# Performance work log

Measured on AMD Instinct MI355X. Metric: run time of the kernel, lower is better.

The kernel has to match this reference:

```python
import jax, jax.numpy as jnp
import numpy as np

N, E = 50000, 800000
IN, HID, H, OUT = 128, 32, 4, 40
K_SAMPLE, EPS_K = 25.0, 1e-3  # fixed k=25 (no dp_budget), compute_beta eps


def _glorot(key, shape):
    fan_in, fan_out = shape[0], shape[-1]
    lim = jnp.sqrt(6.0 / (fan_in + fan_out))
    return jax.random.uniform(key, shape, jnp.float32, -lim, lim)


def setup_inputs() -> dict:
    key = jax.random.key(0)
    ks = jax.random.split(key, 16)
    x = jax.random.normal(ks[0], (N, IN), jnp.float32)
    edge_index = jax.random.randint(ks[1], (2, E), 0, N, jnp.int64)
    # layer 0: IN -> (H, HID)
    W0 = _glorot(ks[2], (IN, H * HID)); as0 = _glorot(ks[3], (H, HID)); ad0 = _glorot(ks[4], (H, HID)); b0 = jnp.zeros((H * HID,), jnp.float32)
    # layer 1: H*HID -> (H, HID)
    W1 = _glorot(ks[5], (H * HID, H * HID)); as1 = _glorot(ks[6], (H, HID)); ad1 = _glorot(ks[7], (H, HID)); b1 = jnp.zeros((H * HID,), jnp.float32)
    # layer 2: H*HID -> (1, OUT)
    W2 = _glorot(ks[8], (H * HID, OUT)); as2 = _glorot(ks[9], (1, OUT)); ad2 = _glorot(ks[10], (1, OUT)); b2 = jnp.zeros((OUT,), jnp.float32)
    # BatchNorm affine params (batch-stat mode, deterministic)
    g_bn0 = jnp.ones((H * HID,), jnp.float32); be_bn0 = jnp.zeros((H * HID,), jnp.float32)
    g_bn1 = jnp.ones((H * HID,), jnp.float32); be_bn1 = jnp.zeros((H * HID,), jnp.float32)
    return {"x": x, "edge_index": edge_index,
            "W0": W0, "as0": as0, "ad0": ad0, "b0": b0,
            "W1": W1, "as1": as1, "ad1": ad1, "b1": b1,
            "W2": W2, "as2": as2, "ad2": ad2, "b2": b2,
            "g_bn0": g_bn0, "be_bn0": be_bn0, "g_bn1": g_bn1, "be_bn1": be_bn1}


def gat_conv(x, src, dst, W, a_src, a_dst, bias, heads, d_out):
    # PyG GATConv, add_self_loops=False, concat over heads
    h = (x @ W).reshape(-1, heads, d_out)                       # [N,H,D]
    al_s = jnp.sum(h * a_src, axis=-1)                          # [N,H]
    al_d = jnp.sum(h * a_dst, axis=-1)                          # [N,H]
    e = jax.nn.leaky_relu(al_s[src] + al_d[dst], 0.2)           # [E,H]
    m = jax.ops.segment_max(e, dst, num_segments=N)
    m = jnp.where(jnp.isfinite(m), m, 0.0)                      # guard empty segments
    p = jnp.exp(e - m[dst])
    s = jax.ops.segment_sum(p, dst, num_segments=N)
    alpha = p / (s[dst] + 1e-16)                                # segment softmax over incoming edges
    out = jax.ops.segment_sum(alpha[:, :, None] * h[src], dst, num_segments=N)  # [N,H,D]
    return out.reshape(-1, heads * d_out) + bias


def batch_norm(x, gamma, beta):
    mu = jnp.mean(x, axis=0)
    var = jnp.mean(jnp.square(x - mu), axis=0)
    return gamma * (x - mu) * jax.lax.rsqrt(var + 1e-5) + beta


def beta_scale(l):
    return 1.0 + 1.0 / (l + 1.0) * (1.0 / (K_SAMPLE + EPS_K))


def reference(x, edge_index, W0, as0, ad0, b0, W1, as1, ad1, b1, W2, as2, ad2, b2,
              g_bn0, be_bn0, g_bn1, be_bn1):
    src, dst = edge_index[0], edge_index[1]
    h = gat_conv(x, src, dst, W0, as0, ad0, b0, H, HID)
    h = jax.nn.elu(batch_norm(h, g_bn0, be_bn0)) * beta_scale(0)
    h = gat_conv(h, src, dst, W1, as1, ad1, b1, H, HID)
    h = jax.nn.elu(batch_norm(h, g_bn1, be_bn1)) * beta_scale(1)
    h = gat_conv(h, src, dst, W2, as2, ad2, b2, 1, OUT)
    return jax.nn.log_softmax(h, axis=1)
```

## Files before the change

### kernel.cpp

```cpp
#include <hip/hip_runtime.h>
#include <math.h>

#define N_NODES 50000
#define N_EDGES 800000
#define DIN 128
#define DHID 128
#define NH 4
#define HID 32
#define DOUT 40

#define PB 128
#define NPB 391

typedef __fp16 fp16x2 __attribute__((ext_vector_type(2)));

static __device__ __forceinline__ float lrelu(float x) { return x > 0.f ? x : 0.2f * x; }

static __device__ __forceinline__ unsigned int pkh(float a, float b) {
    union { fp16x2 h2; unsigned int u; } cv;
    cv.h2 = __builtin_amdgcn_cvt_pkrtz(a, b);
    return cv.u;
}
static __device__ __forceinline__ unsigned short f2h(float a) {
    union { _Float16 h; unsigned short s; } cv;
    cv.h = (_Float16)a;
    return cv.s;
}

static __device__ __forceinline__ void fma8(float* acc, uint4 w, float p) {
    union { unsigned int u; _Float16 h[2]; } c0, c1, c2, c3;
    c0.u = w.x; c1.u = w.y; c2.u = w.z; c3.u = w.w;
    acc[0] = fmaf((float)c0.h[0], p, acc[0]);
    acc[1] = fmaf((float)c0.h[1], p, acc[1]);
    acc[2] = fmaf((float)c1.h[0], p, acc[2]);
    acc[3] = fmaf((float)c1.h[1], p, acc[3]);
    acc[4] = fmaf((float)c2.h[0], p, acc[4]);
    acc[5] = fmaf((float)c2.h[1], p, acc[5]);
    acc[6] = fmaf((float)c3.h[0], p, acc[6]);
    acc[7] = fmaf((float)c3.h[1], p, acc[7]);
}

static __device__ __forceinline__ float4 bnelu4(float4 x, float4 sc, float4 sh, float bs) {
    float y0 = fmaf(x.x, sc.x, sh.x);
    float y1 = fmaf(x.y, sc.y, sh.y);
    float y2 = fmaf(x.z, sc.z, sh.z);
    float y3 = fmaf(x.w, sc.w, sh.w);
    y0 = (y0 > 0.f ? y0 : __expf(y0) - 1.f) * bs;
    y1 = (y1 > 0.f ? y1 : __expf(y1) - 1.f) * bs;
    y2 = (y2 > 0.f ? y2 : __expf(y2) - 1.f) * bs;
    y3 = (y3 > 0.f ? y3 : __expf(y3) - 1.f) * bs;
    return {y0, y1, y2, y3};
}

__global__ __launch_bounds__(256) void bucket_hist_kernel(const int* __restrict__ dstv, int* __restrict__ bhist) {
    __shared__ int h[PB];
    if (threadIdx.x < PB) h[threadIdx.x] = 0;
    __syncthreads();
    for (int i = blockIdx.x * blockDim.x + threadIdx.x; i < N_EDGES; i += gridDim.x * blockDim.x)
        atomicAdd(&h[(unsigned)dstv[i] / NPB], 1);
    __syncthreads();
    if (threadIdx.x < PB) atomicAdd(&bhist[threadIdx.x], h[threadIdx.x]);
}

__global__ __launch_bounds__(128) void bucket_scan_kernel(const int* __restrict__ bhist,
                                                          int* __restrict__ bucket_base, int* __restrict__ cursor) {
    __shared__ int sA[PB], sB[PB];
    int t = threadIdx.x;
    sA[t] = bhist[t];
    __syncthreads();
    int* s = sA; int* d2 = sB;
    for (int off = 1; off < PB; off <<= 1) {
        d2[t] = s[t] + (t >= off ? s[t - off] : 0);
        __syncthreads();
        int* tmp = s; s = d2; d2 = tmp;
    }
    int excl = s[t] - bhist[t];
    bucket_base[t] = excl;
    cursor[t] = excl;
    if (t == PB - 1) bucket_base[PB] = s[t];
}

__global__ __launch_bounds__(256) void partition_kernel(const int* __restrict__ srcv, const int* __restrict__ dstv,
                                                        int* __restrict__ cursor, uint2* __restrict__ part) {
    __shared__ uint2 rec[2048];
    __shared__ int cnt[PB], lofs[PB], gbase[PB];
    __shared__ int sA[PB], sB[PB];
    __shared__ int tot_s;
    const int t = threadIdx.x;
    const int base0 = blockIdx.x * 4096;
    for (int round = 0; round < 2; ++round) {
        int rbase = base0 + round * 2048;
        if (t < PB) cnt[t] = 0;
        __syncthreads();
        int myb[8]; int myr[8]; uint2 myrec[8];
#pragma unroll
        for (int i = 0; i < 8; ++i) {
            int e = rbase + i * 256 + t;
            bool valid = e < N_EDGES;
            int sv = valid ? srcv[e] : 0;
            int dv = valid ? dstv[e] : 0;
            myrec[i].x = (unsigned)sv;
            myrec[i].y = (unsigned)dv;
            int b = (unsigned)dv / NPB;
            myb[i] = valid ? b : -1;
            myr[i] = valid ? atomicAdd(&cnt[b], 1) : 0;
        }
        __syncthreads();
        if (t < PB) sA[t] = cnt[t];
        __syncthreads();
        int* s = sA; int* d2 = sB;
        for (int off = 1; off < PB; off <<= 1) {
            if (t < PB) d2[t] = s[t] + (t >= off ? s[t - off] : 0);
            __syncthreads();
            int* tmp = s; s = d2; d2 = tmp;
        }
        if (t < PB) {
            int c = cnt[t];
            lofs[t] = s[t] - c;
            gbase[t] = c > 0 ? atomicAdd(&cursor[t], c) : 0;
            if (t == PB - 1) tot_s = s[t];
        }
        __syncthreads();
#pragma unroll
        for (int i = 0; i < 8; ++i)
            if (myb[i] >= 0) rec[lofs[myb[i]] + myr[i]] = myrec[i];
        __syncthreads();
        int tot = tot_s;
#pragma unroll
        for (int i = 0; i < 8; ++i) {
            int lp = i * 256 + t;
            if (lp < tot) {
                uint2 r = rec[lp];
                int b = r.y / NPB;
                part[gbase[b] + (lp - lofs[b])] = r;
            }
        }
        __syncthreads();
    }
}

__global__ __launch_bounds__(256) void bucket_csr_kernel(const uint2* __restrict__ part, const int* __restrict__ bucket_base,
                                                         int* __restrict__ row_ptr, int* __restrict__ csr_src) {
    __shared__ int hist[512], sA[512], sB[512], cur[NPB];
    const int b = blockIdx.x, t = threadIdx.x;
    const int base = bucket_base[b];
    const int n = bucket_base[b + 1] - base;
    hist[t] = 0; hist[t + 256] = 0;
    __syncthreads();
    for (int i = t; i < n; i += 256)
        atomicAdd(&hist[part[base + i].y - b * NPB], 1);
    __syncthreads();
    sA[t] = hist[t]; sA[t + 256] = hist[t + 256];
    __syncthreads();
    int* s = sA; int* d2 = sB;
    for (int off = 1; off < 512; off <<= 1) {
        d2[t] = s[t] + (t >= off ? s[t - off] : 0);
        int u = t + 256;
        d2[u] = s[u] + (u >= off ? s[u - off] : 0);
        __syncthreads();
        int* tmp = s; s = d2; d2 = tmp;
    }
    for (int j = t; j < NPB; j += 256) {
        int node = b * NPB + j;
        int excl = s[j] - hist[j];
        if (node < N_NODES) row_ptr[node] = base + excl;
        cur[j] = excl;
    }
    if (b == PB - 1 && t == 0) row_ptr[N_NODES] = N_EDGES;
    __syncthreads();
    for (int i = t; i < n; i += 256) {
        uint2 r = part[base + i];
        int loc = r.y - b * NPB;
        int p = atomicAdd(&cur[loc], 1);
        csr_src[base + p] = (int)r.x;
    }
}

__global__ __launch_bounds__(256) void gemm128_kernel(
    const float* __restrict__ X, const float* __restrict__ W,
    const float* __restrict__ a_src, const float* __restrict__ a_dst,
    const float* __restrict__ scale, const float* __restrict__ shift, float bscale, int apply_bn,
    unsigned int* __restrict__ Hout, float* __restrict__ als, float* __restrict__ ald) {
    __shared__ float Xs[32][68];
    __shared__ float Ws[32][64];
    const int t = threadIdx.x;
    const int tx = t & 15, ty = t >> 4;
    const int r0 = (blockIdx.x >> 1) * 64;
    const int c0 = (blockIdx.x & 1) * 64;
    const int sr = t >> 2, sa = t & 3;
    const int wk = t >> 4, wc = (t & 15) * 4;

    int gr = r0 + sr; gr = gr < N_NODES ? gr : N_NODES - 1;
    const float* Xrow = X + (size_t)gr * 128;
    float4 xpreA = *(const float4*)(Xrow + 8 * sa);
    float4 xpreB = *(const float4*)(Xrow + 8 * sa + 4);
    if (apply_bn) {
        xpreA = bnelu4(xpreA, *(const float4*)(scale + 8 * sa), *(const float4*)(shift + 8 * sa), bscale);
        xpreB = bnelu4(xpreB, *(const float4*)(scale + 8 * sa + 4), *(const float4*)(shift + 8 * sa + 4), bscale);
    }
    float4 wpreA = *(const float4*)(W + (size_t)wk * 128 + c0 + wc);
    float4 wpreB = *(const float4*)(W + (size_t)(wk + 16) * 128 + c0 + wc);

    float acc[4][4];
#pragma unroll
    for (int i = 0; i < 4; ++i)
#pragma unroll
        for (int c = 0; c < 4; ++c) acc[i][c] = 0.f;

    for (int step = 0; step < 4; ++step) {
        __syncthreads();
        Xs[8 * sa + 0][sr] = xpreA.x;
        Xs[8 * sa + 1][sr] = xpreA.y;
        Xs[8 * sa + 2][sr] = xpreA.z;
        Xs[8 * sa + 3][sr] = xpreA.w;
        Xs[8 * sa + 4][sr] = xpreB.x;
        Xs[8 * sa + 5][sr] = xpreB.y;
        Xs[8 * sa + 6][sr] = xpreB.z;
        Xs[8 * sa + 7][sr] = xpreB.w;
        *(float4*)&Ws[wk][wc] = wpreA;
        *(float4*)&Ws[wk + 16][wc] = wpreB;
        if (step < 3) {
            int k0 = (step + 1) * 32;
            xpreA = *(const float4*)(Xrow + k0 + 8 * sa);
            xpreB = *(const float4*)(Xrow + k0 + 8 * sa + 4);
            if (apply_bn) {
                xpreA = bnelu4(xpreA, *(const float4*)(scale + k0 + 8 * sa), *(const float4*)(shift + k0 + 8 * sa), bscale);
                xpreB = bnelu4(xpreB, *(const float4*)(scale + k0 + 8 * sa + 4), *(const float4*)(shift + k0 + 8 * sa + 4), bscale);
            }
            wpreA = *(const float4*)(W + (size_t)(k0 + wk) * 128 + c0 + wc);
            wpreB = *(const float4*)(W + (size_t)(k0 + wk + 16) * 128 + c0 + wc);
        }
        __syncthreads();
#pragma unroll
        for (int kk = 0; kk < 32; ++kk) {
            float4 xv = *(const float4*)&Xs[kk][4 * ty];
            float4 wv = *(const float4*)&Ws[kk][4 * tx];
            float xr[4] = {xv.x, xv.y, xv.z, xv.w};
            float wr[4] = {wv.x, wv.y, wv.z, wv.w};
#pragma unroll
            for (int i = 0; i < 4; ++i)
#pragma unroll
                for (int c = 0; c < 4; ++c)
                    acc[i][c] = fmaf(xr[i], wr[c], acc[i][c]);
        }
    }
    const int head = (c0 >> 5) + (tx >> 3);
    float asv[4], adv[4];
#pragma unroll
    for (int c = 0; c < 4; ++c) {
        asv[c] = a_src[(head & 1) * 32 + (4 * tx + c) % 32 + (head >> 1) * 64];
        adv[c] = a_dst[(head & 1) * 32 + (4 * tx + c) % 32 + (head >> 1) * 64];
    }
#pragma unroll
    for (int i = 0; i < 4; ++i) {
        int r = r0 + 4 * ty + i;
        bool valid = r < N_NODES;
        if (valid) {
            uint2 pk = {pkh(acc[i][0], acc[i][1]), pkh(acc[i][2], acc[i][3])};
            *(uint2*)(Hout + (size_t)r * 64 + (c0 >> 1) + 2 * tx) = pk;
        }
        float ps = 0.f, pd = 0.f;
#pragma unroll
        for (int c = 0; c < 4; ++c) {
            ps = fmaf(acc[i][c], asv[c], ps);
            pd = fmaf(acc[i][c], adv[c], pd);
        }
#pragma unroll
        for (int off = 1; off < 8; off <<= 1) {
            ps += __shfl_xor(ps, off);
            pd += __shfl_xor(pd, off);
        }
        if (valid && (tx & 7) == 0) {
            als[r * 4 + head] = ps;
            ald[r * 4 + head] = pd;
        }
    }
}

__global__ __launch_bounds__(256) void gemm40_kernel(
    const float* __restrict__ X, const float* __restrict__ W,
    const float* __restrict__ a_src, const float* __restrict__ a_dst,
    const float* __restrict__ scale, const float* __restrict__ shift, float bscale,
    unsigned short* __restrict__ Hout, float* __restrict__ als, float* __restrict__ ald) {
    __shared__ float Xs[64][36];
    __shared__ float Ws[40][36];
    const int t = threadIdx.x;
    const int tx = t & 7, ty = t >> 3;
    const int r0 = blockIdx.x * 64;
    const int sr = t >> 2, sa = t & 3;

    int gr = r0 + sr; gr = gr < N_NODES ? gr : N_NODES - 1;
    const float* Xrow = X + (size_t)gr * 128;
    float4 xpreA = bnelu4(*(const float4*)(Xrow + 8 * sa),
                          *(const float4*)(scale + 8 * sa), *(const float4*)(shift + 8 * sa), bscale);
    float4 xpreB = bnelu4(*(const float4*)(Xrow + 8 * sa + 4),
                          *(const float4*)(scale + 8 * sa + 4), *(const float4*)(shift + 8 * sa + 4), bscale);
    float wpre[5];
#pragma unroll
    for (int i = 0; i < 5; ++i) wpre[i] = W[t + 256 * i];

    float acc[2][5];
#pragma unroll
    for (int i = 0; i < 2; ++i)
#pragma unroll
        for (int j = 0; j < 5; ++j) acc[i][j] = 0.f;

    for (int step = 0; step < 4; ++step) {
        __syncthreads();
        *(float4*)&Xs[sr][8 * sa] = xpreA;
        *(float4*)&Xs[sr][8 * sa + 4] = xpreB;
#pragma unroll
        for (int i = 0; i < 5; ++i) {
            int idx = t + 256 * i;
            Ws[idx % 40][idx / 40] = wpre[i];
        }
        if (step < 3) {
            int k0 = (step + 1) * 32;
            xpreA = bnelu4(*(const float4*)(Xrow + k0 + 8 * sa),
                           *(const float4*)(scale + k0 + 8 * sa), *(const float4*)(shift + k0 + 8 * sa), bscale);
            xpreB = bnelu4(*(const float4*)(Xrow + k0 + 8 * sa + 4),
                           *(const float4*)(scale + k0 + 8 * sa + 4), *(const float4*)(shift + k0 + 8 * sa + 4), bscale);
#pragma unroll
            for (int i = 0; i < 5; ++i) wpre[i] = W[k0 * 40 + t + 256 * i];
        }
        __syncthreads();
#pragma unroll
        for (int kk4 = 0; kk4 < 8; ++kk4) {
            float4 xa = *(const float4*)&Xs[2 * ty][4 * kk4];
            float4 xb = *(const float4*)&Xs[2 * ty + 1][4 * kk4];
#pragma unroll
            for (int j = 0; j < 5; ++j) {
                float4 wv = *(const float4*)&Ws[tx + 8 * j][4 * kk4];
                acc[0][j] = fmaf(xa.x, wv.x, acc[0][j]);
                acc[0][j] = fmaf(xa.y, wv.y, acc[0][j]);
                acc[0][j] = fmaf(xa.z, wv.z, acc[0][j]);
                acc[0][j] = fmaf(xa.w, wv.w, acc[0][j]);
                acc[1][j] = fmaf(xb.x, wv.x, acc[1][j]);
                acc[1][j] = fmaf(xb.y, wv.y, acc[1][j]);
                acc[1][j] = fmaf(xb.z, wv.z, acc[1][j]);
                acc[1][j] = fmaf(xb.w, wv.w, acc[1][j]);
            }
        }
    }
    float asv[5], adv[5];
#pragma unroll
    for (int j = 0; j < 5; ++j) {
        asv[j] = a_src[tx + 8 * j];
        adv[j] = a_dst[tx + 8 * j];
    }
#pragma unroll
    for (int i = 0; i < 2; ++i) {
        int r = r0 + 2 * ty + i;
        bool valid = r < N_NODES;
        if (valid) {
#pragma unroll
            for (int j = 0; j < 5; ++j)
                Hout[(size_t)r * 40 + tx + 8 * j] = f2h(acc[i][j]);
        }
        float ps = 0.f, pd = 0.f;
#pragma unroll
        for (int j = 0; j < 5; ++j) {
            ps = fmaf(acc[i][j], asv[j], ps);
            pd = fmaf(acc[i][j], adv[j], pd);
        }
#pragma unroll
        for (int off = 1; off < 8; off <<= 1) {
            ps += __shfl_xor(ps, off);
            pd += __shfl_xor(pd, off);
        }
        if (valid && tx == 0) {
            als[r] = ps;
            ald[r] = pd;
        }
    }
}

__global__ __launch_bounds__(256) void agg128_kernel(
    const int* __restrict__ row_ptr, const int* __restrict__ csr_src,
    const unsigned int* __restrict__ Ht, const float* __restrict__ als, const float* __restrict__ ald,
    const float* __restrict__ bias, float* __restrict__ out) {
    __shared__ float s_p[4][256];
    __shared__ int s_u[4][64];
    int v = (blockIdx.x * blockDim.x + threadIdx.x) >> 6;
    v = __builtin_amdgcn_readfirstlane(v);
    int lane = threadIdx.x & 63;
    int wslot = threadIdx.x >> 6;
    if (v >= N_NODES) return;
    int beg = row_ptr[v], end = row_ptr[v + 1];
    float4 ad4 = *(const float4*)(ald + (size_t)v * 4);
    const int g = lane >> 4;
    const int li = lane & 15;
    const int hh = li >> 2;
    float tsum = 0.f;
    float acc[8];
#pragma unroll
    for (int j = 0; j < 8; ++j) acc[j] = 0.f;

    for (int cbeg = beg; cbeg < end; cbeg += 64) {
        int cnt = min(64, end - cbeg);
        bool act = lane < cnt;
        int u = act ? csr_src[cbeg + lane] : 0;
        float p0, p1, p2, p3;
        if (act) {
            float4 s4 = *(const float4*)(als + (size_t)u * 4);
            p0 = __expf(lrelu(s4.x + ad4.x));
            p1 = __expf(lrelu(s4.y + ad4.y));
            p2 = __expf(lrelu(s4.z + ad4.z));
            p3 = __expf(lrelu(s4.w + ad4.w));
        } else {
            p0 = p1 = p2 = p3 = 0.f;
        }
        s_u[wslot][lane] = u;
        float4 pv = {p0, p1, p2, p3};
        *(float4*)&s_p[wslot][lane * 4] = pv;
        for (int i = 0; i < cnt; i += 4) {
            int e = i + g;
            int uu = s_u[wslot][e];
            float p = s_p[wslot][e * 4 + hh];
            uint4 w4 = *(const uint4*)(Ht + (size_t)uu * 64 + li * 4);
            tsum += p;
            fma8(acc, w4, p);
        }
    }
#pragma unroll
    for (int j = 0; j < 8; ++j) {
        acc[j] += __shfl_xor(acc[j], 16);
        acc[j] += __shfl_xor(acc[j], 32);
    }
    tsum += __shfl_xor(tsum, 16);
    tsum += __shfl_xor(tsum, 32);
    float inv = 1.f / (tsum + 1e-16f);
    if (g == 0) {
        float4 b0 = *(const float4*)(bias + 8 * li);
        float4 b1 = *(const float4*)(bias + 8 * li + 4);
        float4 o0 = {acc[0] * inv + b0.x, acc[1] * inv + b0.y, acc[2] * inv + b0.z, acc[3] * inv + b0.w};
        float4 o1 = {acc[4] * inv + b1.x, acc[5] * inv + b1.y, acc[6] * inv + b1.z, acc[7] * inv + b1.w};
        *(float4*)(out + (size_t)v * DHID + 8 * li) = o0;
        *(float4*)(out + (size_t)v * DHID + 8 * li + 4) = o1;
    }
}

__global__ __launch_bounds__(256) void agg40_kernel(
    const int* __restrict__ row_ptr, const int* __restrict__ csr_src,
    const unsigned int* __restrict__ HtU, const float* __restrict__ als, const float* __restrict__ ald,
    const float* __restrict__ bias, float* __restrict__ out) {
    __shared__ float s_p[4][64];
    __shared__ int s_u[4][64];
    int v = (blockIdx.x * blockDim.x + threadIdx.x) >> 6;
    v = __builtin_amdgcn_readfirstlane(v);
    int lane = threadIdx.x & 63;
    int wslot = threadIdx.x >> 6;
    if (v >= N_NODES) return;
    int beg = row_ptr[v], end = row_ptr[v + 1];
    float adv = ald[v];
    const int g = lane >> 5;
    const int li = lane & 31;
    const bool own = li < 20;
    float tsum = 0.f;
    float a0 = 0.f, a1 = 0.f;
    for (int cbeg = beg; cbeg < end; cbeg += 64) {
        int cnt = min(64, end - cbeg);
        bool act = lane < cnt;
        int u = act ? csr_src[cbeg + lane] : 0;
        float p = act ? __expf(lrelu(als[u] + adv)) : 0.f;
        s_u[wslot][lane] = u;
        s_p[wslot][lane] = p;
        for (int i = 0; i < cnt; i += 2) {
            int e2 = i + g;
            int uu = s_u[wslot][e2];
            float pp = s_p[wslot][e2];
            unsigned int w = own ? HtU[(size_t)uu * 20 + li] : 0u;
            union { unsigned int u; _Float16 h[2]; } cv;
            cv.u = w;
            tsum += pp;
            a0 = fmaf((float)cv.h[0], pp, a0);
            a1 = fmaf((float)cv.h[1], pp, a1);
        }
    }
    a0 += __shfl_xor(a0, 32);
    a1 += __shfl_xor(a1, 32);
    tsum += __shfl_xor(tsum, 32);
    float inv = 1.f / (tsum + 1e-16f);
    float z0 = own ? (a0 * inv + bias[2 * li]) : -1e30f;
    float z1 = own ? (a1 * inv + bias[2 * li + 1]) : -1e30f;
    float zm = fmaxf(z0, z1);
#pragma unroll
    for (int off = 1; off < 32; off <<= 1) zm = fmaxf(zm, __shfl_xor(zm, off));
    float se = own ? (__expf(z0 - zm) + __expf(z1 - zm)) : 0.f;
#pragma unroll
    for (int off = 1; off < 32; off <<= 1) se += __shfl_xor(se, off);
    float ls = zm + logf(se);
    if (own && g == 0) {
        float2 o = {z0 - ls, z1 - ls};
        *(float2*)(out + (size_t)v * DOUT + 2 * li) = o;
    }
}

__global__ __launch_bounds__(256) void bn_stats_kernel(const float* __restrict__ X,
                                                       float* __restrict__ sums, float* __restrict__ sqs) {
    int f = threadIdx.x & 127;
    int sub = threadIdx.x >> 7;
    int rbeg = blockIdx.x * 100;
    float s = 0.f, q = 0.f;
    for (int r = rbeg + sub; r < rbeg + 100; r += 2) {
        float x = X[(size_t)r * DHID + f];
        s += x;
        q += x * x;
    }
    __shared__ float ls[256], lq[256];
    ls[threadIdx.x] = s;
    lq[threadIdx.x] = q;
    __syncthreads();
    if (threadIdx.x < 128) {
        s = ls[threadIdx.x] + ls[threadIdx.x + 128];
        q = lq[threadIdx.x] + lq[threadIdx.x + 128];
        atomicAdd(&sums[f], s);
        atomicAdd(&sqs[f], q);
    }
}

__global__ void bn_finalize_kernel(const float* __restrict__ sums, const float* __restrict__ sqs,
                                   const float* __restrict__ gamma, const float* __restrict__ beta,
                                   float* __restrict__ scale, float* __restrict__ shift) {
    int f = threadIdx.x;
    if (f < DHID) {
        float mu = sums[f] * (1.f / N_NODES);
        float var = sqs[f] * (1.f / N_NODES) - mu * mu;
        float sc = gamma[f] * rsqrtf(var + 1e-5f);
        scale[f] = sc;
        shift[f] = beta[f] - mu * sc;
    }
}

extern "C" void kernel_launch(void* const* d_in, const int* in_sizes, int n_in,
                              void* d_out, int out_size, void* d_ws, size_t ws_size,
                              hipStream_t stream) {
    (void)in_sizes; (void)n_in; (void)out_size; (void)ws_size;
    const float* x = (const float*)d_in[0];
    const int* ei = (const int*)d_in[1];
    const float* W0 = (const float*)d_in[2];
    const float* as0 = (const float*)d_in[3];
    const float* ad0 = (const float*)d_in[4];
    const float* b0 = (const float*)d_in[5];
    const float* W1 = (const float*)d_in[6];
    const float* as1 = (const float*)d_in[7];
    const float* ad1 = (const float*)d_in[8];
    const float* b1 = (const float*)d_in[9];
    const float* W2 = (const float*)d_in[10];
    const float* as2 = (const float*)d_in[11];
    const float* ad2 = (const float*)d_in[12];
    const float* b2 = (const float*)d_in[13];
    const float* g_bn0 = (const float*)d_in[14];
    const float* be_bn0 = (const float*)d_in[15];
    const float* g_bn1 = (const float*)d_in[16];
    const float* be_bn1 = (const float*)d_in[17];
    float* out = (float*)d_out;

    const int* srcv = ei;
    const int* dstv = ei + N_EDGES;

    char* p = (char*)d_ws;
    auto carve = [&](size_t bytes) {
        char* q = p;
        p += (bytes + 255) & ~(size_t)255;
        return q;
    };
    unsigned int* h_bf = (unsigned int*)carve((size_t)N_NODES * 64 * 4);
    float* agg   = (float*)carve((size_t)N_NODES * DHID * 4);
    float* als   = (float*)carve((size_t)N_NODES * NH * 4);
    float* ald   = (float*)carve((size_t)N_NODES * NH * 4);
    int* row_ptr = (int*)carve((size_t)(N_NODES + 1) * 4);
    int* csr_src = (int*)carve((size_t)N_EDGES * 4);
    uint2* part  = (uint2*)carve((size_t)N_EDGES * 8);
    int* bhist   = (int*)carve(PB * 4);
    int* bucket_base = (int*)carve((PB + 1) * 4);
    int* cursor  = (int*)carve(PB * 4);
    float* sums  = (float*)carve(256 * 4);
    float* sqs   = sums + 128;
    float* scale = (float*)carve(DHID * 4);
    float* shift = (float*)carve(DHID * 4);

    const float bs0 = 1.0f + 1.0f / 25.001f;
    const float bs1 = 1.0f + 0.5f / 25.001f;

    const int RT64 = (N_NODES + 63) / 64;
    const int G128B = RT64 * 2;
    const int G40B = RT64;
    const int AB = (N_NODES * 64 + 255) / 256;
    const int PARTB = (N_EDGES + 4095) / 4096;

    hipMemsetAsync(bhist, 0, PB * 4, stream);
    bucket_hist_kernel<<<400, 256, 0, stream>>>(dstv, bhist);
    bucket_scan_kernel<<<1, PB, 0, stream>>>(bhist, bucket_base, cursor);
    partition_kernel<<<PARTB, 256, 0, stream>>>(srcv, dstv, cursor, part);
    bucket_csr_kernel<<<PB, 256, 0, stream>>>(part, bucket_base, row_ptr, csr_src);

    gemm128_kernel<<<G128B, 256, 0, stream>>>(x, W0, as0, ad0, nullptr, nullptr, 1.f, 0, h_bf, als, ald);
    agg128_kernel<<<AB, 256, 0, stream>>>(row_ptr, csr_src, h_bf, als, ald, b0, agg);
    hipMemsetAsync(sums, 0, 256 * 4, stream);
    bn_stats_kernel<<<500, 256, 0, stream>>>(agg, sums, sqs);
    bn_finalize_kernel<<<1, 128, 0, stream>>>(sums, sqs, g_bn0, be_bn0, scale, shift);

    gemm128_kernel<<<G128B, 256, 0, stream>>>(agg, W1, as1, ad1, scale, shift, bs0, 1, h_bf, als, ald);
    agg128_kernel<<<AB, 256, 0, stream>>>(row_ptr, csr_src, h_bf, als, ald, b1, agg);
    hipMemsetAsync(sums, 0, 256 * 4, stream);
    bn_stats_kernel<<<500, 256, 0, stream>>>(agg, sums, sqs);
    bn_finalize_kernel<<<1, 128, 0, stream>>>(sums, sqs, g_bn1, be_bn1, scale, shift);

    gemm40_kernel<<<G40B, 256, 0, stream>>>(agg, W2, as2, ad2, scale, shift, bs1, (unsigned short*)h_bf, als, ald);
    agg40_kernel<<<AB, 256, 0, stream>>>(row_ptr, csr_src, h_bf, als, ald, b2, out);
}
```

Before: 302.2 us.

## Fuse scan and BN finalize via last-block pattern, widen agg40 gathers to uint4

The bucket histogram now runs the prefix scan in whichever block finishes last, and BN stats compute scale/shift the same way from per-block partials. This removes several small kernel launches and memsets, and the float atomics in BN stats become plain stores of partials. agg40 now has 12 edge groups of 5 lanes, each loading a uint4 (8 halves), and reduces the groups through shared memory. In exchange it adds a serial 500-block reduction in one block and a shared-memory reduction at the end of agg40.

```diff
diff --git a/kernel.cpp b/kernel.cpp
--- a/kernel.cpp
+++ b/kernel.cpp
@@ -11,6 +11,7 @@
 
 #define PB 128
 #define NPB 391
+#define BN_BLOCKS 500
 
 typedef __fp16 fp16x2 __attribute__((ext_vector_type(2)));
 
@@ -52,32 +53,40 @@
     return {y0, y1, y2, y3};
 }
 
-__global__ __launch_bounds__(256) void bucket_hist_kernel(const int* __restrict__ dstv, int* __restrict__ bhist) {
+__global__ __launch_bounds__(256) void bucket_hist_scan_kernel(
+    const int* __restrict__ dstv, int* __restrict__ bhist, int* __restrict__ counter,
+    int* __restrict__ bucket_base, int* __restrict__ cursor) {
     __shared__ int h[PB];
-    if (threadIdx.x < PB) h[threadIdx.x] = 0;
-    __syncthreads();
-    for (int i = blockIdx.x * blockDim.x + threadIdx.x; i < N_EDGES; i += gridDim.x * blockDim.x)
+    const int t = threadIdx.x;
+    if (t < PB) h[t] = 0;
+    __syncthreads();
+    for (int i = blockIdx.x * blockDim.x + t; i < N_EDGES; i += gridDim.x * blockDim.x)
         atomicAdd(&h[(unsigned)dstv[i] / NPB], 1);
     __syncthreads();
-    if (threadIdx.x < PB) atomicAdd(&bhist[threadIdx.x], h[threadIdx.x]);
-}
-
-__global__ __launch_bounds__(128) void bucket_scan_kernel(const int* __restrict__ bhist,
-                                                          int* __restrict__ bucket_base, int* __restrict__ cursor) {
-    __shared__ int sA[PB], sB[PB];
-    int t = threadIdx.x;
-    sA[t] = bhist[t];
-    __syncthreads();
-    int* s = sA; int* d2 = sB;
-    for (int off = 1; off < PB; off <<= 1) {
-        d2[t] = s[t] + (t >= off ? s[t - off] : 0);
-        __syncthreads();
-        int* tmp = s; s = d2; d2 = tmp;
-    }
-    int excl = s[t] - bhist[t];
-    bucket_base[t] = excl;
-    cursor[t] = excl;
-    if (t == PB - 1) bucket_base[PB] = s[t];
+    if (t < PB) atomicAdd(&bhist[t], h[t]);
+    __threadfence();
+    __shared__ int done_s;
+    __syncthreads();
+    if (t == 0) done_s = atomicAdd(counter, 1);
+    __syncthreads();
+    if (done_s == gridDim.x - 1) {
+        __threadfence();
+        __shared__ int sA[PB], sB[PB];
+        if (t < PB) sA[t] = bhist[t];
+        __syncthreads();
+        int* s = sA; int* d2 = sB;
+        for (int off = 1; off < PB; off <<= 1) {
+            if (t < PB) d2[t] = s[t] + (t >= off ? s[t - off] : 0);
+            __syncthreads();
+            int* tmp = s; s = d2; d2 = tmp;
+        }
+        if (t < PB) {
+            int excl = s[t] - bhist[t];
+            bucket_base[t] = excl;
+            cursor[t] = excl;
+            if (t == PB - 1) bucket_base[PB] = s[t];
+        }
+    }
 }
 
 __global__ __launch_bounds__(256) void partition_kernel(const int* __restrict__ srcv, const int* __restrict__ dstv,
@@ -442,10 +451,11 @@
 
 __global__ __launch_bounds__(256) void agg40_kernel(
     const int* __restrict__ row_ptr, const int* __restrict__ csr_src,
-    const unsigned int* __restrict__ HtU, const float* __restrict__ als, const float* __restrict__ ald,
+    const uint4* __restrict__ Ht4, const float* __restrict__ als, const float* __restrict__ ald,
     const float* __restrict__ bias, float* __restrict__ out) {
-    __shared__ float s_p[4][64];
-    __shared__ int s_u[4][64];
+    __shared__ float s_p[4][76];
+    __shared__ int s_u[4][76];
+    __shared__ float s_red[4][12][41];
     int v = (blockIdx.x * blockDim.x + threadIdx.x) >> 6;
     v = __builtin_amdgcn_readfirstlane(v);
     int lane = threadIdx.x & 63;
@@ -453,11 +463,15 @@
     if (v >= N_NODES) return;
     int beg = row_ptr[v], end = row_ptr[v + 1];
     float adv = ald[v];
-    const int g = lane >> 5;
-    const int li = lane & 31;
-    const bool own = li < 20;
+    const int g = lane / 5;
+    const int li = lane - g * 5;
+    const bool gact = lane < 60;
+    if (lane < 12) { s_u[wslot][64 + lane] = 0; s_p[wslot][64 + lane] = 0.f; }
     float tsum = 0.f;
-    float a0 = 0.f, a1 = 0.f;
+    float a[8];
+#pragma unroll
+    for (int j = 0; j < 8; ++j) a[j] = 0.f;
+
     for (int cbeg = beg; cbeg < end; cbeg += 64) {
         int cnt = min(64, end - cbeg);
         bool act = lane < cnt;
@@ -465,41 +479,47 @@
         float p = act ? __expf(lrelu(als[u] + adv)) : 0.f;
         s_u[wslot][lane] = u;
         s_p[wslot][lane] = p;
-        for (int i = 0; i < cnt; i += 2) {
-            int e2 = i + g;
-            int uu = s_u[wslot][e2];
-            float pp = s_p[wslot][e2];
-            unsigned int w = own ? HtU[(size_t)uu * 20 + li] : 0u;
-            union { unsigned int u; _Float16 h[2]; } cv;
-            cv.u = w;
-            tsum += pp;
-            a0 = fmaf((float)cv.h[0], pp, a0);
-            a1 = fmaf((float)cv.h[1], pp, a1);
-        }
-    }
-    a0 += __shfl_xor(a0, 32);
-    a1 += __shfl_xor(a1, 32);
-    tsum += __shfl_xor(tsum, 32);
-    float inv = 1.f / (tsum + 1e-16f);
-    float z0 = own ? (a0 * inv + bias[2 * li]) : -1e30f;
-    float z1 = own ? (a1 * inv + bias[2 * li + 1]) : -1e30f;
-    float zm = fmaxf(z0, z1);
-#pragma unroll
-    for (int off = 1; off < 32; off <<= 1) zm = fmaxf(zm, __shfl_xor(zm, off));
-    float se = own ? (__expf(z0 - zm) + __expf(z1 - zm)) : 0.f;
-#pragma unroll
-    for (int off = 1; off < 32; off <<= 1) se += __shfl_xor(se, off);
+        for (int i = 0; i < cnt; i += 12) {
+            int e = i + g;
+            int uu = s_u[wslot][e];
+            float pp = s_p[wslot][e];
+            uint4 w = {0u, 0u, 0u, 0u};
+            if (gact) w = Ht4[(size_t)uu * 5 + li];
+            if (gact) tsum += pp;
+            fma8(a, w, pp);
+        }
+    }
+    if (gact) {
+#pragma unroll
+        for (int j = 0; j < 8; ++j) s_red[wslot][g][li * 8 + j] = a[j];
+        if (li == 0) s_red[wslot][g][40] = tsum;
+    }
+    bool fown = lane < DOUT;
+    float accf = 0.f, T = 0.f;
+#pragma unroll
+    for (int g2 = 0; g2 < 12; ++g2) {
+        if (fown) accf += s_red[wslot][g2][lane];
+        T += s_red[wslot][g2][40];
+    }
+    float inv = 1.f / (T + 1e-16f);
+    float z = fown ? (accf * inv + bias[lane]) : -1e30f;
+    float zm = z;
+#pragma unroll
+    for (int off = 1; off < 64; off <<= 1) zm = fmaxf(zm, __shfl_xor(zm, off));
+    float se = fown ? __expf(z - zm) : 0.f;
+#pragma unroll
+    for (int off = 1; off < 64; off <<= 1) se += __shfl_xor(se, off);
     float ls = zm + logf(se);
-    if (own && g == 0) {
-        float2 o = {z0 - ls, z1 - ls};
-        *(float2*)(out + (size_t)v * DOUT + 2 * li) = o;
-    }
-}
-
-__global__ __launch_bounds__(256) void bn_stats_kernel(const float* __restrict__ X,
-                                                       float* __restrict__ sums, float* __restrict__ sqs) {
-    int f = threadIdx.x & 127;
-    int sub = threadIdx.x >> 7;
+    if (fown) out[(size_t)v * DOUT + lane] = z - ls;
+}
+
+__global__ __launch_bounds__(256) void bn_stats_kernel(
+    const float* __restrict__ X, float* __restrict__ partial, int* __restrict__ counter,
+    const float* __restrict__ gamma, const float* __restrict__ beta,
+    float* __restrict__ scale, float* __restrict__ shift) {
+    const int t = threadIdx.x;
+    int f = t & 127;
+    int sub = t >> 7;
     int rbeg = blockIdx.x * 100;
     float s = 0.f, q = 0.f;
     for (int r = rbeg + sub; r < rbeg + 100; r += 2) {
@@ -508,27 +528,34 @@
         q += x * x;
     }
     __shared__ float ls[256], lq[256];
-    ls[threadIdx.x] = s;
-    lq[threadIdx.x] = q;
-    __syncthreads();
-    if (threadIdx.x < 128) {
-        s = ls[threadIdx.x] + ls[threadIdx.x + 128];
-        q = lq[threadIdx.x] + lq[threadIdx.x + 128];
-        atomicAdd(&sums[f], s);
-        atomicAdd(&sqs[f], q);
-    }
-}
-
-__global__ void bn_finalize_kernel(const float* __restrict__ sums, const float* __restrict__ sqs,
-                                   const float* __restrict__ gamma, const float* __restrict__ beta,
-                                   float* __restrict__ scale, float* __restrict__ shift) {
-    int f = threadIdx.x;
-    if (f < DHID) {
-        float mu = sums[f] * (1.f / N_NODES);
-        float var = sqs[f] * (1.f / N_NODES) - mu * mu;
-        float sc = gamma[f] * rsqrtf(var + 1e-5f);
-        scale[f] = sc;
-        shift[f] = beta[f] - mu * sc;
+    ls[t] = s;
+    lq[t] = q;
+    __syncthreads();
+    if (t < 128) {
+        s = ls[t] + ls[t + 128];
+        q = lq[t] + lq[t + 128];
+        partial[blockIdx.x * 256 + t] = s;
+        partial[blockIdx.x * 256 + 128 + t] = q;
+    }
+    __threadfence();
+    __shared__ int done_s;
+    __syncthreads();
+    if (t == 0) done_s = atomicAdd(counter, 1);
+    __syncthreads();
+    if (done_s == gridDim.x - 1) {
+        __threadfence();
+        if (t < 128) {
+            float S = 0.f, Q = 0.f;
+            for (int b = 0; b < BN_BLOCKS; ++b) {
+                S += partial[b * 256 + t];
+                Q += partial[b * 256 + 128 + t];
+            }
+            float mu = S * (1.f / N_NODES);
+            float var = Q * (1.f / N_NODES) - mu * mu;
+            float sc = gamma[t] * rsqrtf(var + 1e-5f);
+            scale[t] = sc;
+            shift[t] = beta[t] - mu * sc;
+        }
     }
 }
 
@@ -572,11 +599,13 @@
     int* row_ptr = (int*)carve((size_t)(N_NODES + 1) * 4);
     int* csr_src = (int*)carve((size_t)N_EDGES * 4);
     uint2* part  = (uint2*)carve((size_t)N_EDGES * 8);
-    int* bhist   = (int*)carve(PB * 4);
+    int* bhist   = (int*)carve((PB + 8) * 4);
+    int* c_hist  = bhist + PB;
+    int* c_bn0   = bhist + PB + 1;
+    int* c_bn1   = bhist + PB + 2;
     int* bucket_base = (int*)carve((PB + 1) * 4);
     int* cursor  = (int*)carve(PB * 4);
-    float* sums  = (float*)carve(256 * 4);
-    float* sqs   = sums + 128;
+    float* partial = (float*)carve((size_t)BN_BLOCKS * 256 * 4);
     float* scale = (float*)carve(DHID * 4);
     float* shift = (float*)carve(DHID * 4);
 
@@ -589,24 +618,19 @@
     const int AB = (N_NODES * 64 + 255) / 256;
     const int PARTB = (N_EDGES + 4095) / 4096;
 
-    hipMemsetAsync(bhist, 0, PB * 4, stream);
-    bucket_hist_kernel<<<400, 256, 0, stream>>>(dstv, bhist);
-    bucket_scan_kernel<<<1, PB, 0, stream>>>(bhist, bucket_base, cursor);
+    hipMemsetAsync(bhist, 0, (PB + 8) * 4, stream);
+    bucket_hist_scan_kernel<<<400, 256, 0, stream>>>(dstv, bhist, c_hist, bucket_base, cursor);
     partition_kernel<<<PARTB, 256, 0, stream>>>(srcv, dstv, cursor, part);
     bucket_csr_kernel<<<PB, 256, 0, stream>>>(part, bucket_base, row_ptr, csr_src);
 
     gemm128_kernel<<<G128B, 256, 0, stream>>>(x, W0, as0, ad0, nullptr, nullptr, 1.f, 0, h_bf, als, ald);
     agg128_kernel<<<AB, 256, 0, stream>>>(row_ptr, csr_src, h_bf, als, ald, b0, agg);
-    hipMemsetAsync(sums, 0, 256 * 4, stream);
-    bn_stats_kernel<<<500, 256, 0, stream>>>(agg, sums, sqs);
-    bn_finalize_kernel<<<1, 128, 0, stream>>>(sums, sqs, g_bn0, be_bn0, scale, shift);
+    bn_stats_kernel<<<BN_BLOCKS, 256, 0, stream>>>(agg, partial, c_bn0, g_bn0, be_bn0, scale, shift);
 
     gemm128_kernel<<<G128B, 256, 0, stream>>>(agg, W1, as1, ad1, scale, shift, bs0, 1, h_bf, als, ald);
     agg128_kernel<<<AB, 256, 0, stream>>>(row_ptr, csr_src, h_bf, als, ald, b1, agg);
-    hipMemsetAsync(sums, 0, 256 * 4, stream);
-    bn_stats_kernel<<<500, 256, 0, stream>>>(agg, sums, sqs);
-    bn_finalize_kernel<<<1, 128, 0, stream>>>(sums, sqs, g_bn1, be_bn1, scale, shift);
+    bn_stats_kernel<<<BN_BLOCKS, 256, 0, stream>>>(agg, partial, c_bn1, g_bn1, be_bn1, scale, shift);
 
     gemm40_kernel<<<G40B, 256, 0, stream>>>(agg, W2, as2, ad2, scale, shift, bs1, (unsigned short*)h_bf, als, ald);
-    agg40_kernel<<<AB, 256, 0, stream>>>(row_ptr, csr_src, h_bf, als, ald, b2, out);
-}
+    agg40_kernel<<<AB, 256, 0, stream>>>(row_ptr, csr_src, (const uint4*)h_bf, als, ald, b2, out);
+}
```

Result: slower. 387.8 us (+28.3%).
